# Performance work log

Hardware: AMD Instinct MI355X
Metric: run time of the kernel (lower is better)

Reference implementation:

```python
import jax, jax.numpy as jnp
import numpy as np

B = 2; S, H, W = 14, 28, 28; C = 128; NH = 8; WS = 7; SH = 3
N = WS ** 3            # 343 tokens per window
HID = 4 * C            # 512 MLP hidden
EPS = 1e-5
SCALE = (C // NH) ** -0.5


def _rel_index():
    # reproduces the torch code exactly (meshgrid indexing='xy', quirky strides)
    coords = np.stack(np.meshgrid(np.arange(WS), np.arange(WS), np.arange(WS), indexing='xy'))  # (3,7,7,7)
    flat = coords.reshape(3, -1)                              # (3, N)
    rel = flat[:, :, None] - flat[:, None, :]                 # (3, N, N)
    rel = rel.transpose(1, 2, 0).astype(np.int64)             # (N, N, 3)
    rel[..., 0] += WS - 1
    rel[..., 1] += WS - 1
    rel[..., 2] += WS - 1
    rel[..., 0] *= 3 * WS - 1
    rel[..., 1] *= 2 * WS - 1
    return rel.sum(-1)                                        # (N, N)


def _attn_mask():
    # standard shifted-window mask: 0 where same region, -100 otherwise
    img = np.zeros((S, H, W), np.float32)
    sl = (slice(0, -WS), slice(-WS, -SH), slice(-SH, None))
    cnt = 0
    for a in sl:
        for b in sl:
            for c in sl:
                img[a, b, c] = cnt
                cnt += 1
    mw = img.reshape(S // WS, WS, H // WS, WS, W // WS, WS)
    mw = mw.transpose(0, 2, 4, 1, 3, 5).reshape(-1, N)        # (nW, N)
    am = mw[:, None, :] - mw[:, :, None]
    return jnp.asarray(np.where(am != 0, -100.0, 0.0).astype(np.float32))


def setup_inputs() -> dict:
    key = jax.random.key(0)
    ks = jax.random.split(key, 8)
    rn = lambda k, shp, s=0.02: jax.random.normal(k, shp, jnp.float32) * s
    return {
        'x': jax.random.normal(ks[0], (B, S * H * W, C), jnp.float32),
        'mask_matrix': _attn_mask(),
        'g1': jnp.ones((C,), jnp.float32), 'b1': jnp.zeros((C,), jnp.float32),
        'qkv_w': rn(ks[1], (C, 3 * C)), 'qkv_b': jnp.zeros((3 * C,), jnp.float32),
        'rpb': rn(ks[2], ((2 * WS - 1) ** 3, NH)),
        'proj_w': rn(ks[3], (C, C)), 'proj_b': jnp.zeros((C,), jnp.float32),
        'g2': jnp.ones((C,), jnp.float32), 'b2': jnp.zeros((C,), jnp.float32),
        'fc1_w': rn(ks[4], (C, HID)), 'fc1_b': jnp.zeros((HID,), jnp.float32),
        'fc2_w': rn(ks[5], (HID, C)), 'fc2_b': jnp.zeros((C,), jnp.float32),
        'rel_index': jnp.asarray(_rel_index(), jnp.int32),
    }


def _ln(x, g, b):
    mu = x.mean(-1, keepdims=True)
    d = x - mu
    var = (d * d).mean(-1, keepdims=True)
    return d * jax.lax.rsqrt(var + EPS) * g + b


def reference(x, mask_matrix, g1, b1, qkv_w, qkv_b, rpb, proj_w, proj_b,
              g2, b2, fc1_w, fc1_b, fc2_w, fc2_b, rel_index):
    shortcut = x
    h = _ln(x, g1, b1).reshape(B, S, H, W, C)
    h = jnp.roll(h, (-SH, -SH, -SH), axis=(1, 2, 3))
    # window partition -> (B_, N, C)
    h = h.reshape(B, S // WS, WS, H // WS, WS, W // WS, WS, C)
    h = h.transpose(0, 1, 3, 5, 2, 4, 6, 7).reshape(-1, N, C)
    B_ = h.shape[0]
    qkv = (h @ qkv_w + qkv_b).reshape(B_, N, 3, NH, C // NH).transpose(2, 0, 3, 1, 4)
    q, k, v = qkv[0] * SCALE, qkv[1], qkv[2]
    attn = jnp.einsum('bhnd,bhmd->bhnm', q, k)                # (B_, NH, N, N)
    bias = rpb[rel_index.reshape(-1)].reshape(N, N, NH).transpose(2, 0, 1)
    attn = attn + bias[None]
    nW = mask_matrix.shape[0]
    attn = attn.reshape(B_ // nW, nW, NH, N, N) + mask_matrix[None, :, None]
    attn = jax.nn.softmax(attn.reshape(B_, NH, N, N), axis=-1)
    o = jnp.einsum('bhnm,bhmd->bnhd', attn, v).reshape(B_, N, C)
    o = o @ proj_w + proj_b
    # window reverse -> (B, S, H, W, C)
    o = o.reshape(B, S // WS, H // WS, W // WS, WS, WS, WS, C)
    o = o.transpose(0, 1, 4, 2, 5, 3, 6, 7).reshape(B, S, H, W, C)
    o = jnp.roll(o, (SH, SH, SH), axis=(1, 2, 3)).reshape(B, S * H * W, C)
    x = shortcut + o
    y = _ln(x, g2, b2)
    y = jax.nn.gelu(y @ fc1_w + fc1_b, approximate=False) @ fc2_w + fc2_b
    return x + y
```

## Files before the change

kernel.cpp:

```cpp
#include <hip/hip_runtime.h>
#include <hip/hip_bf16.h>
#include <math.h>

typedef _Float16 half2_t __attribute__((ext_vector_type(2)));
typedef _Float16 half4_t __attribute__((ext_vector_type(4)));
typedef _Float16 half8_t __attribute__((ext_vector_type(8)));
typedef float float4_t __attribute__((ext_vector_type(4)));

#define MFMA16(a,b,c) __builtin_amdgcn_mfma_f32_16x16x16f16((a),(b),(c),0,0,0)
#define MFMA32(a,b,c) __builtin_amdgcn_mfma_f32_16x16x32_f16((a),(b),(c),0,0,0)

static __device__ __forceinline__ half2_t cvt_pk(float a, float b) {
  return __builtin_bit_cast(half2_t, __builtin_amdgcn_cvt_pkrtz(a, b));
}

static constexpr int NTOK = 21952;
static constexpr int NREG = 5488;
static constexpr float LOG2E = 1.44269504088896340736f;

__device__ __forceinline__ int rid_of(int cls, int n) {
  int z = n / 49, r = n - z*49, y = r / 7, x = r - y*7;
  int rs = (cls & 4) ? (z < 4 ? 1 : 2) : 0;
  int rh = (cls & 2) ? (y < 4 ? 1 : 2) : 0;
  int rw = (cls & 1) ? (x < 4 ? 1 : 2) : 0;
  return rs*9 + rh*3 + rw;
}

__global__ __launch_bounds__(256) void k_precomp(
    const float* __restrict__ qkv_w, const float* __restrict__ proj_w,
    const float* __restrict__ fc1_w, const float* __restrict__ fc2_w,
    const float* __restrict__ rpb,
    _Float16* __restrict__ qkv_wT, _Float16* __restrict__ proj_wT,
    _Float16* __restrict__ fc1_wT, _Float16* __restrict__ fc2_wT,
    _Float16* __restrict__ biasT, unsigned* __restrict__ bmask)
{
  int i = blockIdx.x * 256 + threadIdx.x;
  if (i < 49152) { int n = i >> 7, k = i & 127; qkv_wT[i] = (_Float16)qkv_w[k*384 + n]; return; }
  i -= 49152;
  if (i < 16384) { int n = i >> 7, k = i & 127; proj_wT[i] = (_Float16)proj_w[k*128 + n]; return; }
  i -= 16384;
  if (i < 65536) { int n = i >> 7, k = i & 127; fc1_wT[i] = (_Float16)fc1_w[k*512 + n]; return; }
  i -= 65536;
  if (i < 65536) { int n = i >> 9, k = i & 511; fc2_wT[i] = (_Float16)fc2_w[k*128 + n]; return; }
  i -= 65536;
  if (i < 8*343*352) {
    int h = i / (343*352); int r = i - h*343*352; int q = r / 352; int k = r - q*352;
    _Float16 v;
    if (k >= 343) v = (_Float16)(-30000.f);
    else {
      int zq = q/49, rq_ = q - zq*49, yq = rq_/7, xq = rq_ - yq*7;
      int zk = k/49, rk_ = k - zk*49, yk = rk_/7, xk = rk_ - yk*7;
      int idx = 20*(yq - yk + 6) + 13*(zq - zk + 6) + (xq - xk + 6);
      v = (_Float16)(rpb[idx*8 + h] * LOG2E);
    }
    biasT[i] = v;
    return;
  }
  i -= 8*343*352;
  if (i < 8*343*11) {
    int cls = i / (343*11); int r = i - cls*343*11; int q = r / 11; int kt = r - q*11;
    int rq = rid_of(cls, q);
    unsigned wbits = 0u;
    for (int j = 0; j < 32; ++j) {
      int k = kt*32 + j;
      if (k < 343 && rid_of(cls, k) == rq) wbits |= (1u << j);
    }
    bmask[i] = wbits;
  }
}

__device__ __forceinline__ void qkv_store(int row, int col, float v,
    const float* __restrict__ bias, _Float16* __restrict__ outh)
{
  v += bias[col];
  int which = col >> 7;
  if (which == 0) v *= 0.25f;
  int hh = (col >> 4) & 7, d = col & 15;
  int w = row / 343, n = row - w*343;
  size_t base = (size_t)((which*64 + w)*8 + hh)*NREG;
  if (which == 2) outh[base + d*343 + n] = (_Float16)v;
  else            outh[base + n*16  + d] = (_Float16)v;
}

__global__ __launch_bounds__(384) void k_qkv(
    const float* __restrict__ x, const float* __restrict__ g1, const float* __restrict__ b1,
    const _Float16* __restrict__ qkv_wT, const float* __restrict__ qkv_b,
    _Float16* __restrict__ qkvb)
{
  __shared__ _Float16 A[32][136];
  int mt = blockIdx.x;
  int tid = threadIdx.x, wid = tid >> 6, lane = tid & 63;
  for (int r = wid; r < 32; r += 6) {
    int row = mt*32 + r;
    int w = row / 343, n = row - w*343;
    int b = w >> 5, widx = w & 31;
    int sz = widx >> 4, sy = (widx >> 2) & 3, sx = widx & 3;
    int z = n / 49, rem = n - z*49, y = rem / 7, xx = rem - y*7;
    int gs = sz*7 + z + 3;  if (gs >= 14) gs -= 14;
    int gh = sy*7 + y + 3;  if (gh >= 28) gh -= 28;
    int gw = sx*7 + xx + 3; if (gw >= 28) gw -= 28;
    int gt = b*10976 + (gs*28 + gh)*28 + gw;
    const float* xr = x + (size_t)gt*128;
    float2 v = *(const float2*)(xr + lane*2);
    float s = v.x + v.y, sq = v.x*v.x + v.y*v.y;
    #pragma unroll
    for (int o = 1; o < 64; o <<= 1) { s += __shfl_xor(s, o); sq += __shfl_xor(sq, o); }
    float mu = s * 0.0078125f;
    float rstd = rsqrtf(sq*0.0078125f - mu*mu + 1e-5f);
    int c = lane*2;
    half2_t hv = { (_Float16)((v.x-mu)*rstd*g1[c]   + b1[c]),
                   (_Float16)((v.y-mu)*rstd*g1[c+1] + b1[c+1]) };
    *(half2_t*)&A[r][c] = hv;
  }
  __syncthreads();
  int lo = lane & 15, grp = lane >> 4;
  const _Float16* bp = qkv_wT + (size_t)(wid*64 + lo)*128 + grp*8;
  float4_t a00={0,0,0,0}, a01={0,0,0,0}, a02={0,0,0,0}, a03={0,0,0,0};
  float4_t a10={0,0,0,0}, a11={0,0,0,0}, a12={0,0,0,0}, a13={0,0,0,0};
  #pragma unroll
  for (int kk = 0; kk < 128; kk += 32) {
    half8_t f0 = *(const half8_t*)&A[lo][kk + grp*8];
    half8_t f1 = *(const half8_t*)&A[16 + lo][kk + grp*8];
    half8_t b0 = *(const half8_t*)(bp + kk);
    half8_t b1 = *(const half8_t*)(bp + kk + (size_t)16*128);
    half8_t b2 = *(const half8_t*)(bp + kk + (size_t)32*128);
    half8_t b3 = *(const half8_t*)(bp + kk + (size_t)48*128);
    a00 = MFMA32(f0, b0, a00);  a01 = MFMA32(f0, b1, a01);
    a02 = MFMA32(f0, b2, a02);  a03 = MFMA32(f0, b3, a03);
    a10 = MFMA32(f1, b0, a10);  a11 = MFMA32(f1, b1, a11);
    a12 = MFMA32(f1, b2, a12);  a13 = MFMA32(f1, b3, a13);
  }
  int row0 = mt*32 + grp*4;
  int colb = wid*64 + lo;
  #pragma unroll
  for (int r = 0; r < 4; ++r) {
    qkv_store(row0+r,    colb,    a00[r], qkv_b, qkvb);
    qkv_store(row0+r,    colb+16, a01[r], qkv_b, qkvb);
    qkv_store(row0+r,    colb+32, a02[r], qkv_b, qkvb);
    qkv_store(row0+r,    colb+48, a03[r], qkv_b, qkvb);
    qkv_store(row0+16+r, colb,    a10[r], qkv_b, qkvb);
    qkv_store(row0+16+r, colb+16, a11[r], qkv_b, qkvb);
    qkv_store(row0+16+r, colb+32, a12[r], qkv_b, qkvb);
    qkv_store(row0+16+r, colb+48, a13[r], qkv_b, qkvb);
  }
}

__global__ __launch_bounds__(512) void k_attn(
    const _Float16* __restrict__ qkv, const _Float16* __restrict__ biasT,
    const unsigned* __restrict__ bmask, _Float16* __restrict__ obuf)
{
  __shared__ _Float16 Klds[352][24];
  __shared__ _Float16 VTlds[16][360];
  int bx = blockIdx.x;
  int w = bx >> 4, h = (bx >> 1) & 7, hf = bx & 1;
  int b = w >> 5, widx = w & 31;
  int sz = widx >> 4, sy = (widx >> 2) & 3, sx = widx & 3;
  int cls = (sz << 2) | (sy == 3 ? 2 : 0) | (sx == 3 ? 1 : 0);
  int tid = threadIdx.x;
  const _Float16* qp  = qkv + (size_t)(w*8 + h) * NREG;
  const _Float16* kp  = qp + (size_t)512  * NREG;
  const _Float16* vtp = qp + (size_t)1024 * NREG;
  for (int c = tid; c < 704; c += 512) {
    int n = c >> 1, d0 = (c & 1) * 8;
    half8_t kv = {};
    if (n < 343) kv = *(const half8_t*)(kp + n*16 + d0);
    *(half8_t*)&Klds[n][d0] = kv;
  }
  for (int c = tid; c < 704; c += 512) {
    int d = c / 44, n0 = (c - d*44) * 8;
    half8_t vv = {};
    if (n0 + 8 <= 343) vv = *(const half8_t*)(vtp + d*343 + n0);
    else { for (int j = 0; j < 8; ++j) vv[j] = (n0 + j < 343) ? vtp[d*343 + n0 + j] : (_Float16)0.f; }
    *(half8_t*)&VTlds[d][n0] = vv;
  }
  __syncthreads();
  int lane = tid & 63, lo = lane & 15, grp = lane >> 4;
  int wid = tid >> 6;
  int qt_end = hf*11 + 11;
  for (int qt = hf*11 + wid; qt < qt_end; qt += 8) {
    int q  = qt*16 + lo;
    int qv = q < 343 ? q : 342;
    half4_t qf = *(const half4_t*)(qp + (size_t)qv*16 + grp*4);
    const _Float16* bp  = biasT + (size_t)(h*343 + qv)*352;
    const unsigned* bmp = bmask + (size_t)(cls*343 + qv)*11;
    half4_t barr0[11], barr1[11];
    unsigned bmarr[11];
    #pragma unroll
    for (int kt = 0; kt < 11; ++kt) {
      barr0[kt] = *(const half4_t*)(bp + kt*32 + grp*4);
      barr1[kt] = *(const half4_t*)(bp + kt*32 + 16 + grp*4);
      bmarr[kt] = bmp[kt];
    }
    float lsum = 0.f;
    float4_t acc = {0.f, 0.f, 0.f, 0.f};
    #pragma unroll
    for (int kt = 0; kt < 11; ++kt) {
      int kb = kt*32;
      half4_t ka0 = *(const half4_t*)&Klds[kb + lo][grp*4];
      half4_t ka1 = *(const half4_t*)&Klds[kb + 16 + lo][grp*4];
      float4_t zero = {0.f, 0.f, 0.f, 0.f};
      float4_t s0 = MFMA16(ka0, qf, zero);
      float4_t s1 = MFMA16(ka1, qf, zero);
      unsigned bmw = bmarr[kt];
      float p[8];
      #pragma unroll
      for (int i = 0; i < 8; ++i) {
        float sv = (i < 4) ? s0[i] : s1[i-4];
        float bb = (float)((i < 4) ? barr0[kt][i] : barr1[kt][i-4]);
        float e = exp2f(fmaf(sv, LOG2E, bb));
        unsigned bit = (bmw >> ((i >> 2)*16 + grp*4 + (i & 3))) & 1u;
        p[i] = bit ? e : 0.f;
        lsum += p[i];
      }
      half2_t pk01 = cvt_pk(p[0], p[1]);
      half2_t pk23 = cvt_pk(p[2], p[3]);
      half2_t pk45 = cvt_pk(p[4], p[5]);
      half2_t pk67 = cvt_pk(p[6], p[7]);
      half4_t pb0 = __builtin_shufflevector(pk01, pk23, 0, 1, 2, 3);
      half4_t pb1 = __builtin_shufflevector(pk45, pk67, 0, 1, 2, 3);
      half4_t va0 = *(const half4_t*)&VTlds[lo][kb + grp*4];
      half4_t va1 = *(const half4_t*)&VTlds[lo][kb + 16 + grp*4];
      acc = MFMA16(va0, pb0, acc);
      acc = MFMA16(va1, pb1, acc);
    }
    lsum += __shfl_xor(lsum, 16);
    lsum += __shfl_xor(lsum, 32);
    if (q < 343) {
      int z = q/49, rem = q - z*49, y = rem/7, xx = rem - y*7;
      int gs = sz*7 + z + 3;  if (gs >= 14) gs -= 14;
      int gh = sy*7 + y + 3;  if (gh >= 28) gh -= 28;
      int gw = sx*7 + xx + 3; if (gw >= 28) gw -= 28;
      int gt = b*10976 + (gs*28 + gh)*28 + gw;
      float rl = 1.f / lsum;
      half4_t o4 = { (_Float16)(acc[0]*rl), (_Float16)(acc[1]*rl),
                     (_Float16)(acc[2]*rl), (_Float16)(acc[3]*rl) };
      *(half4_t*)(obuf + (size_t)gt*128 + h*16 + grp*4) = o4;
    }
  }
}

__global__ __launch_bounds__(512, 4) void k_mlp(
    const _Float16* __restrict__ obuf, const _Float16* __restrict__ proj_wT,
    const float* __restrict__ proj_b, const float* __restrict__ x,
    const float* __restrict__ g2, const float* __restrict__ b2,
    const _Float16* __restrict__ fc1_wT, const float* __restrict__ fc1_b,
    const _Float16* __restrict__ fc2_wT, const float* __restrict__ fc2_b,
    float* __restrict__ out)
{
  __shared__ _Float16 P[32][136];
  __shared__ _Float16 X2[32][136];
  __shared__ _Float16 H[32][520];
  int mt = blockIdx.x;
  int row0b = mt*32;
  int tid = threadIdx.x, wid = tid >> 6, lane = tid & 63, lo = lane & 15, grp = lane >> 4;
  {
    const _Float16* bp = proj_wT + (size_t)(wid*16 + lo)*128 + grp*8;
    const _Float16* ap0 = obuf + (size_t)(row0b + lo)*128 + grp*8;
    const _Float16* ap1 = ap0 + (size_t)16*128;
    half8_t wreg[4];
    #pragma unroll
    for (int k4 = 0; k4 < 4; ++k4) wreg[k4] = *(const half8_t*)(bp + k4*32);
    #pragma unroll
    for (int k4 = 0; k4 < 4; ++k4) asm volatile("" :: "v"(wreg[k4]));
    float4_t a0={0,0,0,0}, a1={0,0,0,0};
    #pragma unroll
    for (int k4 = 0; k4 < 4; ++k4) {
      half8_t f0 = *(const half8_t*)(ap0 + k4*32);
      half8_t f1 = *(const half8_t*)(ap1 + k4*32);
      a0 = MFMA32(f0, wreg[k4], a0);
      a1 = MFMA32(f1, wreg[k4], a1);
    }
    int colb = wid*16 + lo;
    float bb = proj_b[colb];
    #pragma unroll
    for (int r = 0; r < 4; ++r) {
      int r0 = grp*4 + r;
      int row0 = row0b + r0, row1 = row0 + 16;
      X2[r0][colb]    = (_Float16)(x[(size_t)row0*128 + colb] + a0[r] + bb);
      X2[r0+16][colb] = (_Float16)(x[(size_t)row1*128 + colb] + a1[r] + bb);
    }
  }
  __syncthreads();
  for (int r = wid; r < 32; r += 8) {
    half2_t hx = *(const half2_t*)&X2[r][lane*2];
    float2 v = { (float)hx[0], (float)hx[1] };
    float s = v.x + v.y, sq = v.x*v.x + v.y*v.y;
    #pragma unroll
    for (int o = 1; o < 64; o <<= 1) { s += __shfl_xor(s, o); sq += __shfl_xor(sq, o); }
    float mu = s * 0.0078125f;
    float rstd = rsqrtf(sq*0.0078125f - mu*mu + 1e-5f);
    int c = lane*2;
    half2_t hv = { (_Float16)((v.x-mu)*rstd*g2[c]   + b2[c]),
                   (_Float16)((v.y-mu)*rstd*g2[c+1] + b2[c+1]) };
    *(half2_t*)&P[r][c] = hv;
  }
  __syncthreads();
  {
    const _Float16* bp = fc1_wT + (size_t)(wid*64 + lo)*128 + grp*8;
    half8_t w1[4][4];
    #pragma unroll
    for (int k4 = 0; k4 < 4; ++k4)
      #pragma unroll
      for (int j = 0; j < 4; ++j)
        w1[k4][j] = *(const half8_t*)(bp + k4*32 + (size_t)(j*16)*128);
    #pragma unroll
    for (int k4 = 0; k4 < 4; ++k4)
      #pragma unroll
      for (int j = 0; j < 4; ++j)
        asm volatile("" :: "v"(w1[k4][j]));
    float4_t a00={0,0,0,0}, a01={0,0,0,0}, a02={0,0,0,0}, a03={0,0,0,0};
    float4_t a10={0,0,0,0}, a11={0,0,0,0}, a12={0,0,0,0}, a13={0,0,0,0};
    #pragma unroll
    for (int k4 = 0; k4 < 4; ++k4) {
      half8_t f0 = *(const half8_t*)&P[lo][k4*32 + grp*8];
      half8_t f1 = *(const half8_t*)&P[16 + lo][k4*32 + grp*8];
      a00 = MFMA32(f0, w1[k4][0], a00);  a01 = MFMA32(f0, w1[k4][1], a01);
      a02 = MFMA32(f0, w1[k4][2], a02);  a03 = MFMA32(f0, w1[k4][3], a03);
      a10 = MFMA32(f1, w1[k4][0], a10);  a11 = MFMA32(f1, w1[k4][1], a11);
      a12 = MFMA32(f1, w1[k4][2], a12);  a13 = MFMA32(f1, w1[k4][3], a13);
    }
    int colb = wid*64 + lo;
    #pragma unroll
    for (int r = 0; r < 4; ++r) {
      float vv[8] = { a00[r], a01[r], a02[r], a03[r], a10[r], a11[r], a12[r], a13[r] };
      #pragma unroll
      for (int j = 0; j < 8; ++j) {
        int rr  = grp*4 + r + (j >= 4 ? 16 : 0);
        int col = colb + (j & 3)*16;
        float v = vv[j] + fc1_b[col];
        float g = 0.5f * v * (1.0f + erff(v * 0.70710678118654752f));
        H[rr][col] = (_Float16)g;
      }
    }
  }
  __syncthreads();
  {
    const _Float16* bp = fc2_wT + (size_t)(wid*16 + lo)*512 + grp*8;
    half8_t w2[16];
    #pragma unroll
    for (int k = 0; k < 16; ++k) w2[k] = *(const half8_t*)(bp + k*32);
    #pragma unroll
    for (int k = 0; k < 16; ++k) asm volatile("" :: "v"(w2[k]));
    float4_t c0={0,0,0,0}, c1={0,0,0,0};
    #pragma unroll
    for (int k = 0; k < 16; ++k) {
      half8_t f0 = *(const half8_t*)&H[lo][k*32 + grp*8];
      half8_t f1 = *(const half8_t*)&H[16 + lo][k*32 + grp*8];
      c0 = MFMA32(f0, w2[k], c0);
      c1 = MFMA32(f1, w2[k], c1);
    }
    int colb = wid*16 + lo;
    float bb = fc2_b[colb];
    #pragma unroll
    for (int r = 0; r < 4; ++r) {
      int r0 = grp*4 + r;
      int row0 = row0b + r0;
      out[(size_t)row0*128 + colb]      = (float)X2[r0][colb]    + c0[r] + bb;
      out[(size_t)(row0+16)*128 + colb] = (float)X2[r0+16][colb] + c1[r] + bb;
    }
  }
}

extern "C" void kernel_launch(void* const* d_in, const int* in_sizes, int n_in,
                              void* d_out, int out_size, void* d_ws, size_t ws_size,
                              hipStream_t stream)
{
  const float* x      = (const float*)d_in[0];
  const float* g1     = (const float*)d_in[2];
  const float* b1     = (const float*)d_in[3];
  const float* qkv_w  = (const float*)d_in[4];
  const float* qkv_b  = (const float*)d_in[5];
  const float* rpb    = (const float*)d_in[6];
  const float* proj_w = (const float*)d_in[7];
  const float* proj_b = (const float*)d_in[8];
  const float* g2     = (const float*)d_in[9];
  const float* b2     = (const float*)d_in[10];
  const float* fc1_w  = (const float*)d_in[11];
  const float* fc1_b  = (const float*)d_in[12];
  const float* fc2_w  = (const float*)d_in[13];
  const float* fc2_b  = (const float*)d_in[14];
  char* ws = (char*)d_ws;
  size_t o = 0;
  auto alloc = [&](size_t bytes) { size_t r = o; o += (bytes + 255) & ~size_t(255); return r; };
  size_t oOB  = alloc((size_t)NTOK*128*2);
  size_t oU   = alloc((size_t)NTOK*512*2);
  size_t oWQ  = alloc(49152*2);
  size_t oWP  = alloc(16384*2);
  size_t oW1  = alloc(65536*2);
  size_t oW2  = alloc(65536*2);
  size_t oBT  = alloc((size_t)8*343*352*2);
  size_t oBM  = alloc((size_t)8*343*11*4);
  (void)ws_size; (void)in_sizes; (void)n_in; (void)out_size;
  _Float16* obuf   = (_Float16*)(ws + oOB);
  _Float16* qkvb   = (_Float16*)(ws + oU);
  _Float16* qkv_wT = (_Float16*)(ws + oWQ);
  _Float16* proj_wT= (_Float16*)(ws + oWP);
  _Float16* fc1_wT = (_Float16*)(ws + oW1);
  _Float16* fc2_wT = (_Float16*)(ws + oW2);
  _Float16* biasT  = (_Float16*)(ws + oBT);
  unsigned* bmask  = (unsigned*)(ws + oBM);
  float*    out    = (float*)d_out;

  k_precomp<<<4662, 256, 0, stream>>>(qkv_w, proj_w, fc1_w, fc2_w, rpb,
                                      qkv_wT, proj_wT, fc1_wT, fc2_wT, biasT, bmask);
  k_qkv<<<686, 384, 0, stream>>>(x, g1, b1, qkv_wT, qkv_b, qkvb);
  k_attn<<<1024, 512, 0, stream>>>(qkvb, biasT, bmask, obuf);
  k_mlp<<<686, 512, 0, stream>>>(obuf, proj_wT, proj_b, x, g2, b2,
                                 fc1_wT, fc1_b, fc2_wT, fc2_b, out);
}
```

Measured before the change: 118.5 us.

## Fold log2e into Q scale, feed bias via MFMA accumulator, one block per head

Q is pre-scaled by log2e in the QKV store, and the relative-position bias (already in log2 units) is passed as the MFMA accumulator input. This removes the per-element fma and bias add, leaving only exp2 and masking in the softmax loop. The attention launch also drops from two blocks per (window, head) to one, so each block covers all 22 query tiles. K/V are staged into LDS half as often, but the grid shrinks to 512 blocks and each wave handles about three tiles, which may hurt latency hiding.

```diff
diff --git a/kernel.cpp b/kernel.cpp
--- a/kernel.cpp
+++ b/kernel.cpp
@@ -74,7 +74,7 @@
 {
   v += bias[col];
   int which = col >> 7;
-  if (which == 0) v *= 0.25f;
+  if (which == 0) v *= 0.25f * LOG2E;
   int hh = (col >> 4) & 7, d = col & 15;
   int w = row / 343, n = row - w*343;
   size_t base = (size_t)((which*64 + w)*8 + hh)*NREG;
@@ -152,7 +152,7 @@
   __shared__ _Float16 Klds[352][24];
   __shared__ _Float16 VTlds[16][360];
   int bx = blockIdx.x;
-  int w = bx >> 4, h = (bx >> 1) & 7, hf = bx & 1;
+  int w = bx >> 3, h = bx & 7;
   int b = w >> 5, widx = w & 31;
   int sz = widx >> 4, sy = (widx >> 2) & 3, sx = widx & 3;
   int cls = (sz << 2) | (sy == 3 ? 2 : 0) | (sx == 3 ? 1 : 0);
@@ -176,8 +176,7 @@
   __syncthreads();
   int lane = tid & 63, lo = lane & 15, grp = lane >> 4;
   int wid = tid >> 6;
-  int qt_end = hf*11 + 11;
-  for (int qt = hf*11 + wid; qt < qt_end; qt += 8) {
+  for (int qt = wid; qt < 22; qt += 8) {
     int q  = qt*16 + lo;
     int qv = q < 343 ? q : 342;
     half4_t qf = *(const half4_t*)(qp + (size_t)qv*16 + grp*4);
@@ -198,19 +197,22 @@
       int kb = kt*32;
       half4_t ka0 = *(const half4_t*)&Klds[kb + lo][grp*4];
       half4_t ka1 = *(const half4_t*)&Klds[kb + 16 + lo][grp*4];
-      float4_t zero = {0.f, 0.f, 0.f, 0.f};
-      float4_t s0 = MFMA16(ka0, qf, zero);
-      float4_t s1 = MFMA16(ka1, qf, zero);
-      unsigned bmw = bmarr[kt];
+      float4_t bc0 = { (float)barr0[kt][0], (float)barr0[kt][1],
+                       (float)barr0[kt][2], (float)barr0[kt][3] };
+      float4_t bc1 = { (float)barr1[kt][0], (float)barr1[kt][1],
+                       (float)barr1[kt][2], (float)barr1[kt][3] };
+      float4_t s0 = MFMA16(ka0, qf, bc0);
+      float4_t s1 = MFMA16(ka1, qf, bc1);
+      unsigned m0 = bmarr[kt] >> (grp*4);
+      unsigned m1 = bmarr[kt] >> (16 + grp*4);
       float p[8];
       #pragma unroll
-      for (int i = 0; i < 8; ++i) {
-        float sv = (i < 4) ? s0[i] : s1[i-4];
-        float bb = (float)((i < 4) ? barr0[kt][i] : barr1[kt][i-4]);
-        float e = exp2f(fmaf(sv, LOG2E, bb));
-        unsigned bit = (bmw >> ((i >> 2)*16 + grp*4 + (i & 3))) & 1u;
-        p[i] = bit ? e : 0.f;
-        lsum += p[i];
+      for (int i = 0; i < 4; ++i) {
+        float e0 = exp2f(s0[i]);
+        float e1 = exp2f(s1[i]);
+        p[i]   = (m0 & (1u << i)) ? e0 : 0.f;
+        p[i+4] = (m1 & (1u << i)) ? e1 : 0.f;
+        lsum += p[i] + p[i+4];
       }
       half2_t pk01 = cvt_pk(p[0], p[1]);
       half2_t pk23 = cvt_pk(p[2], p[3]);
@@ -404,7 +406,7 @@
   k_precomp<<<4662, 256, 0, stream>>>(qkv_w, proj_w, fc1_w, fc2_w, rpb,
                                       qkv_wT, proj_wT, fc1_wT, fc2_wT, biasT, bmask);
   k_qkv<<<686, 384, 0, stream>>>(x, g1, b1, qkv_wT, qkv_b, qkvb);
-  k_attn<<<1024, 512, 0, stream>>>(qkvb, biasT, bmask, obuf);
+  k_attn<<<512, 512, 0, stream>>>(qkvb, biasT, bmask, obuf);
   k_mlp<<<686, 512, 0, stream>>>(obuf, proj_wT, proj_b, x, g2, b2,
                                  fc1_wT, fc1_b, fc2_wT, fc2_b, out);
 }
```

New measurement: 115.9 us. 2.2% less time.
